# Optimization experiments

Measured on AMD Instinct MI355X. Metric: run time of the kernel, lower is better.

Reference implementation:

```python
import jax, jax.numpy as jnp
import numpy as np

NUM_GROUPS = 4
DIVERSITY_STRENGTH = -0.5  # module stores negated strength
DIVERSITY_DISCOUNT = 0.5
CANDIDATE_MULTIPLE = 1


def setup_inputs() -> dict:
    key = jax.random.key(0)
    k1, k2, k3 = jax.random.split(key, 3)
    bsz, beam, vocab, nstep = 64, 8, 50257, 5
    return {
        "lprobs": jax.random.normal(k1, (bsz, beam, vocab), dtype=jnp.float32),
        "scores": jax.random.normal(k2, (bsz, beam, nstep), dtype=jnp.float32),
        "group_overlap": jax.random.uniform(k3, (bsz, NUM_GROUPS, NUM_GROUPS), dtype=jnp.float32),
        "mask": jnp.ones((bsz, beam), dtype=jnp.int32),
        "original_batch_idxs": jnp.arange(bsz, dtype=jnp.int64),
        "step": 5,
    }


def reference(lprobs, scores, group_overlap, mask, original_batch_idxs, step):
    # step > 0 path of DiverseBeamSearch.step
    bsz, beam, vocab = lprobs.shape
    G = NUM_GROUPS
    sub = beam // G
    k = sub * CANDIDATE_MULTIPLE
    barange = jnp.arange(bsz)
    go_b = group_overlap[original_batch_idxs]  # (bsz, G, G), pre-update overlap state

    scores_G, beams_G, idx_G = [], [], []
    for g in range(G):
        lp = lprobs[:, g::G, :]                 # (bsz, sub, vocab)
        m_g = mask[:, g::G]                     # (bsz, sub)
        if g > 0:
            idx_prev = jnp.stack(idx_G, axis=-1)            # (bsz, k, g)
            pen = 1.0 + go_b[:, g, :g]                      # (bsz, g)
            src = jnp.broadcast_to(pen[:, None, :], idx_prev.shape).reshape(bsz, -1)
            div = jnp.zeros((bsz, vocab), lprobs.dtype).at[
                barange[:, None], idx_prev.reshape(bsz, -1)
            ].add(src)                                       # scatter_add diversity counts
            lp = lp + DIVERSITY_STRENGTH * div[:, None, :]
        # BeamSearch.step: mask finished beams to 0, add running scores, topk
        lp = jnp.where(m_g[:, :, None] == 0, jnp.asarray(0.0, lp.dtype), lp)
        lp = lp + scores[:, g::G, step - 1][:, :, None]
        vals, flat_idx = jax.lax.top_k(lp.reshape(bsz, sub * vocab), k)
        beams = flat_idx // vocab
        toks = flat_idx % vocab
        scores_G.append(vals)
        beams_G.append(beams * G + g)
        idx_G.append(toks)

    idx_stack = jnp.stack(idx_G, axis=-1)                   # (bsz, k, G)
    scores_buf = jnp.stack(scores_G, axis=2).reshape(bsz, -1)
    indices_buf = idx_stack.reshape(bsz, -1)
    beams_buf = jnp.stack(beams_G, axis=2).reshape(bsz, -1)

    # pairwise token-overlap between groups
    overlap = (idx_stack[:, :, None, :] == idx_stack[:, :, :, None]).astype(jnp.int32)  # (bsz,k,G,G)
    mg = mask.reshape(bsz, -1, G)
    om = mg[:, :, None, :] & mg[:, :, :, None]
    overlap = jnp.where(om == 0, 0, overlap)
    overlap = overlap.sum(axis=1)                            # (bsz, G, G)

    new_group_overlap = group_overlap.at[original_batch_idxs].add(
        overlap.astype(group_overlap.dtype)
    ) * DIVERSITY_DISCOUNT
    return scores_buf, indices_buf, beams_buf, new_group_overlap
```

## Files before the change

### kernel.cpp

```cpp
#include <hip/hip_runtime.h>
#include <limits.h>
#include <math.h>

#define VOCAB 50257
#define BSZ 64
#define BEAM 8
#define NG 4
#define NSTEP 5
#define BLK 256
#define NB 4
#define CHA ((VOCAB + NB - 1) / NB)
#define NROWS (BSZ * BEAM)
#define CANDS_PER_ROW (NB * 8)

struct Cand { float v; int i; };

__device__ __forceinline__ bool pref(float av, int ai, float bv, int bi) {
    return (av > bv) || (av == bv && ai < bi);
}
__device__ __forceinline__ void ce(float& a, int& ia, float& b, int& ib) {
    if (pref(b, ib, a, ia)) { float tv = a; int ti = ia; a = b; ia = ib; b = tv; ib = ti; }
}
__device__ __forceinline__ void hc(float& a, int& ia, float b, int ib) {
    if (pref(b, ib, a, ia)) { a = b; ia = ib; }
}
__device__ __forceinline__ void merge2(float& v0, int& i0, float& v1, int& i1,
                                       float bv0, int bi0, float bv1, int bi1) {
    if (pref(bv0, bi0, v0, i0)) {
        float nv1; int ni1;
        if (pref(v0, i0, bv1, bi1)) { nv1 = v0; ni1 = i0; } else { nv1 = bv1; ni1 = bi1; }
        v0 = bv0; i0 = bi0; v1 = nv1; i1 = ni1;
    } else if (pref(bv0, bi0, v1, i1)) {
        v1 = bv0; i1 = bi0;
    }
}

#define SORT8() do { \
    ce(v0,i0,v4,i4); ce(v1,i1,v5,i5); ce(v2,i2,v6,i6); ce(v3,i3,v7,i7); \
    ce(v0,i0,v2,i2); ce(v1,i1,v3,i3); ce(v4,i4,v6,i6); ce(v5,i5,v7,i7); \
    ce(v0,i0,v1,i1); ce(v2,i2,v3,i3); ce(v4,i4,v5,i5); ce(v6,i6,v7,i7); \
} while (0)

#define INS(T, FI) do { float _t = (T); int _f = (FI); \
    if (pref(_t, _f, v7, i7)) { v7 = _t; i7 = _f; \
        ce(v6,i6,v7,i7); ce(v5,i5,v6,i6); ce(v4,i4,v5,i5); ce(v3,i3,v4,i4); \
        ce(v2,i2,v3,i3); ce(v1,i1,v2,i2); ce(v0,i0,v1,i1); } \
} while (0)

#define WMERGE(OFF) do { \
    float pv0=__shfl_down(v0,OFF), pv1=__shfl_down(v1,OFF), pv2=__shfl_down(v2,OFF), pv3=__shfl_down(v3,OFF); \
    float pv4=__shfl_down(v4,OFF), pv5=__shfl_down(v5,OFF), pv6=__shfl_down(v6,OFF), pv7=__shfl_down(v7,OFF); \
    int   pi0=__shfl_down(i0,OFF), pi1=__shfl_down(i1,OFF), pi2=__shfl_down(i2,OFF), pi3=__shfl_down(i3,OFF); \
    int   pi4=__shfl_down(i4,OFF), pi5=__shfl_down(i5,OFF), pi6=__shfl_down(i6,OFF), pi7=__shfl_down(i7,OFF); \
    hc(v0,i0,pv7,pi7); hc(v1,i1,pv6,pi6); hc(v2,i2,pv5,pi5); hc(v3,i3,pv4,pi4); \
    hc(v4,i4,pv3,pi3); hc(v5,i5,pv2,pi2); hc(v6,i6,pv1,pi1); hc(v7,i7,pv0,pi0); \
    SORT8(); \
} while (0)

#define LMERGE(W) do { \
    float pv0=swv[W][0], pv1=swv[W][1], pv2=swv[W][2], pv3=swv[W][3]; \
    float pv4=swv[W][4], pv5=swv[W][5], pv6=swv[W][6], pv7=swv[W][7]; \
    int   pi0=swi[W][0], pi1=swi[W][1], pi2=swi[W][2], pi3=swi[W][3]; \
    int   pi4=swi[W][4], pi5=swi[W][5], pi6=swi[W][6], pi7=swi[W][7]; \
    hc(v0,i0,pv7,pi7); hc(v1,i1,pv6,pi6); hc(v2,i2,pv5,pi5); hc(v3,i3,pv4,pi4); \
    hc(v4,i4,pv3,pi3); hc(v5,i5,pv2,pi2); hc(v6,i6,pv1,pi1); hc(v7,i7,pv0,pi0); \
    SORT8(); \
} while (0)

__global__ __launch_bounds__(BLK)
void topk_kernel(const float* __restrict__ lprobs, const float* __restrict__ scores,
                 const int* __restrict__ mask, const int* __restrict__ step_p,
                 Cand* __restrict__ cand)
{
    const int tid = threadIdx.x;
    const int bid = blockIdx.x;
    const int r   = bid / NB;
    const int blk = bid % NB;

    const size_t row_off = (size_t)r * VOCAB;
    const float* p       = lprobs + row_off;
    const float  maskf   = mask[r] ? 1.0f : 0.0f;
    const float  sc      = scores[r * NSTEP + (step_p[0] - 1)];
    const int    fb      = ((r & 7) >> 2) * VOCAB;

    int c0 = blk * CHA;
    int c1 = c0 + CHA; if (c1 > VOCAB) c1 = VOCAB;
    const int a  = (int)(row_off & 3);
    int al = c0 + ((4 - ((a + c0) & 3)) & 3); if (al > c1) al = c1;
    const int vend = al + ((c1 - al) & ~3);

    float v0=-INFINITY,v1=-INFINITY,v2=-INFINITY,v3=-INFINITY,
          v4=-INFINITY,v5=-INFINITY,v6=-INFINITY,v7=-INFINITY;
    int   i0=INT_MAX,i1=INT_MAX,i2=INT_MAX,i3=INT_MAX,
          i4=INT_MAX,i5=INT_MAX,i6=INT_MAX,i7=INT_MAX;

    for (int v = c0 + tid; v < al; v += BLK) {
        float t = fmaf(maskf, p[v], sc);
        INS(t, fb + v);
    }
    int v = al + tid * 4;
    if (v < vend) {
        float4 cur = *reinterpret_cast<const float4*>(p + v);
        for (int vn = v + BLK * 4; vn < vend; vn += BLK * 4) {
            float4 nxt = *reinterpret_cast<const float4*>(p + vn);
            INS(fmaf(maskf, cur.x, sc), fb + v);
            INS(fmaf(maskf, cur.y, sc), fb + v + 1);
            INS(fmaf(maskf, cur.z, sc), fb + v + 2);
            INS(fmaf(maskf, cur.w, sc), fb + v + 3);
            cur = nxt; v = vn;
        }
        INS(fmaf(maskf, cur.x, sc), fb + v);
        INS(fmaf(maskf, cur.y, sc), fb + v + 1);
        INS(fmaf(maskf, cur.z, sc), fb + v + 2);
        INS(fmaf(maskf, cur.w, sc), fb + v + 3);
    }
    for (int vv = vend + tid; vv < c1; vv += BLK) {
        float t = fmaf(maskf, p[vv], sc);
        INS(t, fb + vv);
    }

    WMERGE(32); WMERGE(16); WMERGE(8); WMERGE(4); WMERGE(2); WMERGE(1);

    __shared__ float swv[4][8];
    __shared__ int   swi[4][8];
    const int wave = tid >> 6, lane = tid & 63;
    if (lane == 0 && wave > 0) {
        swv[wave][0]=v0; swv[wave][1]=v1; swv[wave][2]=v2; swv[wave][3]=v3;
        swv[wave][4]=v4; swv[wave][5]=v5; swv[wave][6]=v6; swv[wave][7]=v7;
        swi[wave][0]=i0; swi[wave][1]=i1; swi[wave][2]=i2; swi[wave][3]=i3;
        swi[wave][4]=i4; swi[wave][5]=i5; swi[wave][6]=i6; swi[wave][7]=i7;
    }
    __syncthreads();
    if (tid == 0) {
        LMERGE(1); LMERGE(2); LMERGE(3);
        Cand* o = cand + (size_t)bid * 8;
        o[0].v=v0; o[0].i=i0; o[1].v=v1; o[1].i=i1;
        o[2].v=v2; o[2].i=i2; o[3].v=v3; o[3].i=i3;
        o[4].v=v4; o[4].i=i4; o[5].v=v5; o[5].i=i5;
        o[6].v=v6; o[6].i=i6; o[7].v=v7; o[7].i=i7;
    }
}

__global__ __launch_bounds__(64)
void select_kernel(const float* __restrict__ go, const int* __restrict__ mask,
                   const Cand* __restrict__ cand, float* __restrict__ out)
{
    const int b = blockIdx.x, t = threadIdx.x;
    __shared__ float cval[NG][2];
    __shared__ int   ctok[NG][2];
    __shared__ int   cbeam[NG][2];

    const int h = t >> 5;
    const int c = t & 31;

    for (int g = 0; g < NG; ++g) {
        const int s   = g + h * NG;
        const int row = b * BEAM + s;
        const Cand cd = cand[(size_t)row * CANDS_PER_ROW + c];
        float val = cd.v;
        const int fi  = cd.i;
        const int tok = fi - h * VOCAB;
        if (g > 0 && mask[row]) {
            for (int gp = 0; gp < g; ++gp) {
                const float pen = 0.5f * (1.0f + go[b * (NG * NG) + g * NG + gp]);
                if (tok == ctok[gp][0]) val -= pen;
                if (tok == ctok[gp][1]) val -= pen;
            }
        }
        float a0 = val, a1 = -INFINITY; int j0 = fi, j1 = INT_MAX;
        #pragma unroll
        for (int off = 32; off > 0; off >>= 1) {
            float q0 = __shfl_down(a0, off), q1 = __shfl_down(a1, off);
            int   k0 = __shfl_down(j0, off), k1 = __shfl_down(j1, off);
            merge2(a0, j0, a1, j1, q0, k0, q1, k1);
        }
        if (t == 0) {
            const int h0 = (j0 >= VOCAB) ? 1 : 0;
            const int h1 = (j1 >= VOCAB) ? 1 : 0;
            cval[g][0] = a0;               cval[g][1] = a1;
            ctok[g][0] = j0 - h0 * VOCAB;  ctok[g][1] = j1 - h1 * VOCAB;
            cbeam[g][0] = h0 * NG + g;     cbeam[g][1] = h1 * NG + g;
        }
        __syncthreads();
    }

    float* out_scores = out;
    float* out_idx    = out + 512;
    float* out_bms    = out + 1024;
    float* out_go     = out + 1536;

    if (t < 8) {
        const int rank = t >> 2, g = t & 3;
        out_scores[b * 8 + t] = cval[g][rank];
        out_idx[b * 8 + t]    = (float)ctok[g][rank];
        out_bms[b * 8 + t]    = (float)cbeam[g][rank];
    }
    if (t < 16) {
        const int g1 = t >> 2, g2 = t & 3;
        int ov = 0;
        #pragma unroll
        for (int jj = 0; jj < 2; ++jj) {
            const int m1 = mask[b * BEAM + jj * NG + g1];
            const int m2 = mask[b * BEAM + jj * NG + g2];
            if (m1 && m2 && ctok[g1][jj] == ctok[g2][jj]) ++ov;
        }
        out_go[b * (NG * NG) + t] = (go[b * (NG * NG) + t] + (float)ov) * 0.5f;
    }
}

extern "C" void kernel_launch(void* const* d_in, const int* in_sizes, int n_in,
                              void* d_out, int out_size, void* d_ws, size_t ws_size,
                              hipStream_t stream) {
    const float* lprobs = (const float*)d_in[0];
    const float* scores = (const float*)d_in[1];
    const float* go     = (const float*)d_in[2];
    const int*   mask   = (const int*)d_in[3];
    const int*   step_p = (const int*)d_in[5];

    Cand*  cand = (Cand*)d_ws;
    float* out  = (float*)d_out;

    topk_kernel<<<dim3(NROWS * NB), dim3(BLK), 0, stream>>>(lprobs, scores, mask, step_p, cand);
    select_kernel<<<dim3(BSZ), dim3(64), 0, stream>>>(go, mask, cand, out);
}
```

Measured before the change: 183.0 us.

## Replace per-element top-8 insertion with threshold prepass and ballot-compacted candidate filter

The single-pass kernel, which kept a sorted top-8 per thread with index tie-breaks, is replaced by three kernels. A row-max pass computes per-thread maxima and keeps the top 8 of them per block, which gives a safe lower bound for the row's 8th-largest value. A filter pass rereads lprobs and uses wave ballots and atomics to append only elements at or above that bound to a per-row list. The select kernel then applies mask and score to the small list and runs the existing group/diversity selection. This swaps heavy per-element compare-exchange work for a second read of lprobs and atomics. It also relies on filtering raw values before masking, which gives wrong results for masked rows whose values all become equal, and it drops candidates if a list overflows CAP.

Result: slower. 188.2 us (+2.8%).

```diff
diff --git a/kernel.cpp b/kernel.cpp
--- a/kernel.cpp
+++ b/kernel.cpp
@@ -11,9 +11,24 @@
 #define NB 4
 #define CHA ((VOCAB + NB - 1) / NB)
 #define NROWS (BSZ * BEAM)
-#define CANDS_PER_ROW (NB * 8)
+#define NBLKS (NROWS * NB)
+#define CAP 1024
 
 struct Cand { float v; int i; };
+
+#define CEV(a, b) do { float _t = fmaxf(a, b); b = fminf(a, b); a = _t; } while (0)
+#define SORT8V() do { \
+    CEV(w0,w4); CEV(w1,w5); CEV(w2,w6); CEV(w3,w7); \
+    CEV(w0,w2); CEV(w1,w3); CEV(w4,w6); CEV(w5,w7); \
+    CEV(w0,w1); CEV(w2,w3); CEV(w4,w5); CEV(w6,w7); } while (0)
+#define XMERGEV(OFF) do { \
+    float p0=__shfl_xor(w0,OFF), p1=__shfl_xor(w1,OFF), p2=__shfl_xor(w2,OFF), p3=__shfl_xor(w3,OFF); \
+    float p4=__shfl_xor(w4,OFF), p5=__shfl_xor(w5,OFF), p6=__shfl_xor(w6,OFF), p7=__shfl_xor(w7,OFF); \
+    w0=fmaxf(w0,p7); w1=fmaxf(w1,p6); w2=fmaxf(w2,p5); w3=fmaxf(w3,p4); \
+    w4=fmaxf(w4,p3); w5=fmaxf(w5,p2); w6=fmaxf(w6,p1); w7=fmaxf(w7,p0); \
+    SORT8V(); } while (0)
+#define INSV(T) do { float _t = (T); if (_t > w7) { w7 = _t; \
+    CEV(w6,w7); CEV(w5,w6); CEV(w4,w5); CEV(w3,w4); CEV(w2,w3); CEV(w1,w2); CEV(w0,w1); } } while (0)
 
 __device__ __forceinline__ bool pref(float av, int ai, float bv, int bi) {
     return (av > bv) || (av == bv && ai < bi);
@@ -34,152 +49,196 @@
         v1 = bv0; i1 = bi0;
     }
 }
-
-#define SORT8() do { \
+#define SORT8P() do { \
     ce(v0,i0,v4,i4); ce(v1,i1,v5,i5); ce(v2,i2,v6,i6); ce(v3,i3,v7,i7); \
     ce(v0,i0,v2,i2); ce(v1,i1,v3,i3); ce(v4,i4,v6,i6); ce(v5,i5,v7,i7); \
-    ce(v0,i0,v1,i1); ce(v2,i2,v3,i3); ce(v4,i4,v5,i5); ce(v6,i6,v7,i7); \
-} while (0)
-
-#define INS(T, FI) do { float _t = (T); int _f = (FI); \
+    ce(v0,i0,v1,i1); ce(v2,i2,v3,i3); ce(v4,i4,v5,i5); ce(v6,i6,v7,i7); } while (0)
+#define INSP(T, FI) do { float _t = (T); int _f = (FI); \
     if (pref(_t, _f, v7, i7)) { v7 = _t; i7 = _f; \
         ce(v6,i6,v7,i7); ce(v5,i5,v6,i6); ce(v4,i4,v5,i5); ce(v3,i3,v4,i4); \
-        ce(v2,i2,v3,i3); ce(v1,i1,v2,i2); ce(v0,i0,v1,i1); } \
-} while (0)
-
-#define WMERGE(OFF) do { \
-    float pv0=__shfl_down(v0,OFF), pv1=__shfl_down(v1,OFF), pv2=__shfl_down(v2,OFF), pv3=__shfl_down(v3,OFF); \
-    float pv4=__shfl_down(v4,OFF), pv5=__shfl_down(v5,OFF), pv6=__shfl_down(v6,OFF), pv7=__shfl_down(v7,OFF); \
-    int   pi0=__shfl_down(i0,OFF), pi1=__shfl_down(i1,OFF), pi2=__shfl_down(i2,OFF), pi3=__shfl_down(i3,OFF); \
-    int   pi4=__shfl_down(i4,OFF), pi5=__shfl_down(i5,OFF), pi6=__shfl_down(i6,OFF), pi7=__shfl_down(i7,OFF); \
+        ce(v2,i2,v3,i3); ce(v1,i1,v2,i2); ce(v0,i0,v1,i1); } } while (0)
+#define XMERGEP(OFF) do { \
+    float pv0=__shfl_xor(v0,OFF), pv1=__shfl_xor(v1,OFF), pv2=__shfl_xor(v2,OFF), pv3=__shfl_xor(v3,OFF); \
+    float pv4=__shfl_xor(v4,OFF), pv5=__shfl_xor(v5,OFF), pv6=__shfl_xor(v6,OFF), pv7=__shfl_xor(v7,OFF); \
+    int   pi0=__shfl_xor(i0,OFF), pi1=__shfl_xor(i1,OFF), pi2=__shfl_xor(i2,OFF), pi3=__shfl_xor(i3,OFF); \
+    int   pi4=__shfl_xor(i4,OFF), pi5=__shfl_xor(i5,OFF), pi6=__shfl_xor(i6,OFF), pi7=__shfl_xor(i7,OFF); \
     hc(v0,i0,pv7,pi7); hc(v1,i1,pv6,pi6); hc(v2,i2,pv5,pi5); hc(v3,i3,pv4,pi4); \
     hc(v4,i4,pv3,pi3); hc(v5,i5,pv2,pi2); hc(v6,i6,pv1,pi1); hc(v7,i7,pv0,pi0); \
-    SORT8(); \
-} while (0)
-
-#define LMERGE(W) do { \
-    float pv0=swv[W][0], pv1=swv[W][1], pv2=swv[W][2], pv3=swv[W][3]; \
-    float pv4=swv[W][4], pv5=swv[W][5], pv6=swv[W][6], pv7=swv[W][7]; \
-    int   pi0=swi[W][0], pi1=swi[W][1], pi2=swi[W][2], pi3=swi[W][3]; \
-    int   pi4=swi[W][4], pi5=swi[W][5], pi6=swi[W][6], pi7=swi[W][7]; \
-    hc(v0,i0,pv7,pi7); hc(v1,i1,pv6,pi6); hc(v2,i2,pv5,pi5); hc(v3,i3,pv4,pi4); \
-    hc(v4,i4,pv3,pi3); hc(v5,i5,pv2,pi2); hc(v6,i6,pv1,pi1); hc(v7,i7,pv0,pi0); \
-    SORT8(); \
-} while (0)
+    SORT8P(); } while (0)
+
+__device__ __forceinline__ void chunk_ranges(int r, int blk, int& c0, int& c1,
+                                             int& al, int& vend) {
+    c0 = blk * CHA;
+    c1 = c0 + CHA; if (c1 > VOCAB) c1 = VOCAB;
+    const size_t row_off = (size_t)r * VOCAB;
+    const int a = (int)(row_off & 3);
+    al = c0 + ((4 - ((a + c0) & 3)) & 3); if (al > c1) al = c1;
+    vend = al + ((c1 - al) & ~3);
+}
 
 __global__ __launch_bounds__(BLK)
-void topk_kernel(const float* __restrict__ lprobs, const float* __restrict__ scores,
-                 const int* __restrict__ mask, const int* __restrict__ step_p,
-                 Cand* __restrict__ cand)
-{
-    const int tid = threadIdx.x;
-    const int bid = blockIdx.x;
-    const int r   = bid / NB;
-    const int blk = bid % NB;
-
-    const size_t row_off = (size_t)r * VOCAB;
-    const float* p       = lprobs + row_off;
-    const float  maskf   = mask[r] ? 1.0f : 0.0f;
-    const float  sc      = scores[r * NSTEP + (step_p[0] - 1)];
-    const int    fb      = ((r & 7) >> 2) * VOCAB;
-
-    int c0 = blk * CHA;
-    int c1 = c0 + CHA; if (c1 > VOCAB) c1 = VOCAB;
-    const int a  = (int)(row_off & 3);
-    int al = c0 + ((4 - ((a + c0) & 3)) & 3); if (al > c1) al = c1;
-    const int vend = al + ((c1 - al) & ~3);
+void rowmax_kernel(const float* __restrict__ lprobs, float* __restrict__ blk8,
+                   int* __restrict__ counters)
+{
+    const int tid = threadIdx.x, bid = blockIdx.x;
+    if (bid < NROWS && tid == 0) counters[bid] = 0;
+    const int r = bid / NB, blk = bid % NB;
+    const float* p = lprobs + (size_t)r * VOCAB;
+
+    int c0, c1, al, vend;
+    chunk_ranges(r, blk, c0, c1, al, vend);
+
+    float m = -INFINITY;
+    for (int v = c0 + tid; v < al; v += BLK) m = fmaxf(m, p[v]);
+    for (int v = al + tid * 4; v < vend; v += BLK * 4) {
+        const float4 f = *reinterpret_cast<const float4*>(p + v);
+        m = fmaxf(m, fmaxf(fmaxf(f.x, f.y), fmaxf(f.z, f.w)));
+    }
+    for (int v = vend + tid; v < c1; v += BLK) m = fmaxf(m, p[v]);
+
+    float w0 = m, w1 = -INFINITY, w2 = -INFINITY, w3 = -INFINITY,
+          w4 = -INFINITY, w5 = -INFINITY, w6 = -INFINITY, w7 = -INFINITY;
+    XMERGEV(32); XMERGEV(16); XMERGEV(8); XMERGEV(4); XMERGEV(2); XMERGEV(1);
+
+    __shared__ float sw[4][8];
+    const int wave = tid >> 6, lane = tid & 63;
+    if (lane == 0) {
+        sw[wave][0]=w0; sw[wave][1]=w1; sw[wave][2]=w2; sw[wave][3]=w3;
+        sw[wave][4]=w4; sw[wave][5]=w5; sw[wave][6]=w6; sw[wave][7]=w7;
+    }
+    __syncthreads();
+    if (tid == 0) {
+        #pragma unroll
+        for (int w = 1; w < 4; ++w) {
+            INSV(sw[w][0]); INSV(sw[w][1]); INSV(sw[w][2]); INSV(sw[w][3]);
+            INSV(sw[w][4]); INSV(sw[w][5]); INSV(sw[w][6]); INSV(sw[w][7]);
+        }
+        float* o = blk8 + (size_t)bid * 8;
+        o[0]=w0; o[1]=w1; o[2]=w2; o[3]=w3; o[4]=w4; o[5]=w5; o[6]=w6; o[7]=w7;
+    }
+}
+
+__device__ __forceinline__ void append(bool prd, float val, int fi, int row,
+                                       int* __restrict__ counters,
+                                       Cand* __restrict__ lists)
+{
+    unsigned long long mk = __ballot(prd ? 1 : 0);
+    if (mk == 0) return;
+    const int lane = threadIdx.x & 63;
+    const int leader = __ffsll((unsigned long long)mk) - 1;
+    int base = 0;
+    if (lane == leader) base = atomicAdd(&counters[row], __popcll(mk));
+    base = __shfl(base, leader);
+    if (prd) {
+        const int pos = base + __popcll(mk & ((1ull << lane) - 1ull));
+        if (pos < CAP) { Cand c; c.v = val; c.i = fi; lists[(size_t)row * CAP + pos] = c; }
+    }
+}
+
+__global__ __launch_bounds__(BLK)
+void filter_kernel(const float* __restrict__ lprobs, const float* __restrict__ blk8,
+                   int* __restrict__ counters, Cand* __restrict__ lists)
+{
+    const int tid = threadIdx.x, bid = blockIdx.x;
+    const int r = bid / NB, blk = bid % NB;
+    const float* p = lprobs + (size_t)r * VOCAB;
+    const int fb = ((r & 7) >> 2) * VOCAB;
+
+    const int lane = tid & 63;
+    float w0 = (lane < 32) ? blk8[(size_t)(r * NB + (lane >> 3)) * 8 + (lane & 7)]
+                           : -INFINITY;
+    float w1=-INFINITY,w2=-INFINITY,w3=-INFINITY,w4=-INFINITY,w5=-INFINITY,w6=-INFINITY,w7=-INFINITY;
+    XMERGEV(32); XMERGEV(16); XMERGEV(8); XMERGEV(4); XMERGEV(2); XMERGEV(1);
+    const float R8 = w7;
+
+    int c0, c1, al, vend;
+    chunk_ranges(r, blk, c0, c1, al, vend);
+
+    for (int v = c0 + tid; v < al; v += BLK) {
+        const float x = p[v];
+        append(x >= R8, x, fb + v, r, counters, lists);
+    }
+    for (int v = al + tid * 4; v < vend; v += BLK * 4) {
+        const float4 f = *reinterpret_cast<const float4*>(p + v);
+        const float mx = fmaxf(fmaxf(f.x, f.y), fmaxf(f.z, f.w));
+        if (__any(mx >= R8)) {
+            append(f.x >= R8, f.x, fb + v,     r, counters, lists);
+            append(f.y >= R8, f.y, fb + v + 1, r, counters, lists);
+            append(f.z >= R8, f.z, fb + v + 2, r, counters, lists);
+            append(f.w >= R8, f.w, fb + v + 3, r, counters, lists);
+        }
+    }
+    for (int v = vend + tid; v < c1; v += BLK) {
+        const float x = p[v];
+        append(x >= R8, x, fb + v, r, counters, lists);
+    }
+}
+
+__global__ __launch_bounds__(64)
+void select_kernel(const float* __restrict__ scores, const float* __restrict__ go,
+                   const int* __restrict__ mask, const int* __restrict__ step_p,
+                   const int* __restrict__ counters, const Cand* __restrict__ lists,
+                   float* __restrict__ out)
+{
+    const int b = blockIdx.x, t = threadIdx.x;
+    const int rg = t >> 3;
+    const int lc = t & 7;
+    const int row = b * BEAM + rg;
+    const float maskf = mask[row] ? 1.0f : 0.0f;
+    const float sc = scores[row * NSTEP + (step_p[0] - 1)];
+    int n = counters[row]; if (n > CAP) n = CAP;
 
     float v0=-INFINITY,v1=-INFINITY,v2=-INFINITY,v3=-INFINITY,
           v4=-INFINITY,v5=-INFINITY,v6=-INFINITY,v7=-INFINITY;
     int   i0=INT_MAX,i1=INT_MAX,i2=INT_MAX,i3=INT_MAX,
           i4=INT_MAX,i5=INT_MAX,i6=INT_MAX,i7=INT_MAX;
-
-    for (int v = c0 + tid; v < al; v += BLK) {
-        float t = fmaf(maskf, p[v], sc);
-        INS(t, fb + v);
-    }
-    int v = al + tid * 4;
-    if (v < vend) {
-        float4 cur = *reinterpret_cast<const float4*>(p + v);
-        for (int vn = v + BLK * 4; vn < vend; vn += BLK * 4) {
-            float4 nxt = *reinterpret_cast<const float4*>(p + vn);
-            INS(fmaf(maskf, cur.x, sc), fb + v);
-            INS(fmaf(maskf, cur.y, sc), fb + v + 1);
-            INS(fmaf(maskf, cur.z, sc), fb + v + 2);
-            INS(fmaf(maskf, cur.w, sc), fb + v + 3);
-            cur = nxt; v = vn;
-        }
-        INS(fmaf(maskf, cur.x, sc), fb + v);
-        INS(fmaf(maskf, cur.y, sc), fb + v + 1);
-        INS(fmaf(maskf, cur.z, sc), fb + v + 2);
-        INS(fmaf(maskf, cur.w, sc), fb + v + 3);
-    }
-    for (int vv = vend + tid; vv < c1; vv += BLK) {
-        float t = fmaf(maskf, p[vv], sc);
-        INS(t, fb + vv);
-    }
-
-    WMERGE(32); WMERGE(16); WMERGE(8); WMERGE(4); WMERGE(2); WMERGE(1);
-
-    __shared__ float swv[4][8];
-    __shared__ int   swi[4][8];
-    const int wave = tid >> 6, lane = tid & 63;
-    if (lane == 0 && wave > 0) {
-        swv[wave][0]=v0; swv[wave][1]=v1; swv[wave][2]=v2; swv[wave][3]=v3;
-        swv[wave][4]=v4; swv[wave][5]=v5; swv[wave][6]=v6; swv[wave][7]=v7;
-        swi[wave][0]=i0; swi[wave][1]=i1; swi[wave][2]=i2; swi[wave][3]=i3;
-        swi[wave][4]=i4; swi[wave][5]=i5; swi[wave][6]=i6; swi[wave][7]=i7;
+    for (int k = lc; k < n; k += 8) {
+        const Cand cd = lists[(size_t)row * CAP + k];
+        INSP(fmaf(maskf, cd.v, sc), cd.i);
+    }
+    XMERGEP(4); XMERGEP(2); XMERGEP(1);
+
+    __shared__ float cv[BEAM][8];
+    __shared__ int   ci[BEAM][8];
+    if (lc == 0) {
+        cv[rg][0]=v0; cv[rg][1]=v1; cv[rg][2]=v2; cv[rg][3]=v3;
+        cv[rg][4]=v4; cv[rg][5]=v5; cv[rg][6]=v6; cv[rg][7]=v7;
+        ci[rg][0]=i0; ci[rg][1]=i1; ci[rg][2]=i2; ci[rg][3]=i3;
+        ci[rg][4]=i4; ci[rg][5]=i5; ci[rg][6]=i6; ci[rg][7]=i7;
     }
     __syncthreads();
-    if (tid == 0) {
-        LMERGE(1); LMERGE(2); LMERGE(3);
-        Cand* o = cand + (size_t)bid * 8;
-        o[0].v=v0; o[0].i=i0; o[1].v=v1; o[1].i=i1;
-        o[2].v=v2; o[2].i=i2; o[3].v=v3; o[3].i=i3;
-        o[4].v=v4; o[4].i=i4; o[5].v=v5; o[5].i=i5;
-        o[6].v=v6; o[6].i=i6; o[7].v=v7; o[7].i=i7;
-    }
-}
-
-__global__ __launch_bounds__(64)
-void select_kernel(const float* __restrict__ go, const int* __restrict__ mask,
-                   const Cand* __restrict__ cand, float* __restrict__ out)
-{
-    const int b = blockIdx.x, t = threadIdx.x;
+
     __shared__ float cval[NG][2];
     __shared__ int   ctok[NG][2];
     __shared__ int   cbeam[NG][2];
-
-    const int h = t >> 5;
-    const int c = t & 31;
-
     for (int g = 0; g < NG; ++g) {
-        const int s   = g + h * NG;
-        const int row = b * BEAM + s;
-        const Cand cd = cand[(size_t)row * CANDS_PER_ROW + c];
-        float val = cd.v;
-        const int fi  = cd.i;
-        const int tok = fi - h * VOCAB;
-        if (g > 0 && mask[row]) {
-            for (int gp = 0; gp < g; ++gp) {
-                const float pen = 0.5f * (1.0f + go[b * (NG * NG) + g * NG + gp]);
-                if (tok == ctok[gp][0]) val -= pen;
-                if (tok == ctok[gp][1]) val -= pen;
+        float val = -INFINITY; int fi = INT_MAX;
+        if (t < 16) {
+            const int h = t >> 3, c = t & 7;
+            const int s = g + h * NG;
+            val = cv[s][c]; fi = ci[s][c];
+            const int tok = fi - h * VOCAB;
+            if (g > 0 && mask[b * BEAM + s]) {
+                for (int gp = 0; gp < g; ++gp) {
+                    const float pen = 0.5f * (1.0f + go[b * (NG * NG) + g * NG + gp]);
+                    if (tok == ctok[gp][0]) val -= pen;
+                    if (tok == ctok[gp][1]) val -= pen;
+                }
             }
         }
         float a0 = val, a1 = -INFINITY; int j0 = fi, j1 = INT_MAX;
         #pragma unroll
         for (int off = 32; off > 0; off >>= 1) {
-            float q0 = __shfl_down(a0, off), q1 = __shfl_down(a1, off);
-            int   k0 = __shfl_down(j0, off), k1 = __shfl_down(j1, off);
+            const float q0 = __shfl_down(a0, off), q1 = __shfl_down(a1, off);
+            const int   k0 = __shfl_down(j0, off), k1 = __shfl_down(j1, off);
             merge2(a0, j0, a1, j1, q0, k0, q1, k1);
         }
         if (t == 0) {
             const int h0 = (j0 >= VOCAB) ? 1 : 0;
             const int h1 = (j1 >= VOCAB) ? 1 : 0;
-            cval[g][0] = a0;               cval[g][1] = a1;
-            ctok[g][0] = j0 - h0 * VOCAB;  ctok[g][1] = j1 - h1 * VOCAB;
-            cbeam[g][0] = h0 * NG + g;     cbeam[g][1] = h1 * NG + g;
+            cval[g][0] = a0;              cval[g][1] = a1;
+            ctok[g][0] = j0 - h0 * VOCAB; ctok[g][1] = j1 - h1 * VOCAB;
+            cbeam[g][0] = h0 * NG + g;    cbeam[g][1] = h1 * NG + g;
         }
         __syncthreads();
     }
@@ -217,9 +276,13 @@
     const int*   mask   = (const int*)d_in[3];
     const int*   step_p = (const int*)d_in[5];
 
-    Cand*  cand = (Cand*)d_ws;
-    float* out  = (float*)d_out;
-
-    topk_kernel<<<dim3(NROWS * NB), dim3(BLK), 0, stream>>>(lprobs, scores, mask, step_p, cand);
-    select_kernel<<<dim3(BSZ), dim3(64), 0, stream>>>(go, mask, cand, out);
-}
+    float* blk8     = (float*)d_ws;
+    int*   counters = (int*)((char*)d_ws + 65536);
+    Cand*  lists    = (Cand*)((char*)d_ws + 65536 + 2048);
+    float* out      = (float*)d_out;
+
+    rowmax_kernel<<<dim3(NBLKS), dim3(BLK), 0, stream>>>(lprobs, blk8, counters);
+    filter_kernel<<<dim3(NBLKS), dim3(BLK), 0, stream>>>(lprobs, blk8, counters, lists);
+    select_kernel<<<dim3(BSZ), dim3(64), 0, stream>>>(scores, go, mask, step_p,
+                                                      counters, lists, out);
+}
```
